# Performance work log

Hardware: AMD Instinct MI355X
Metric: run time of the kernel (lower is better)

The kernel has to match this reference:

```python
import jax, jax.numpy as jnp
import numpy as np

N_NODES = 50000
N_EDGES = 800000
IN_DIM = 128
IN_CH = 64
HIDDEN = 64
OUT_CH = 128
NUM_CLS = 16
NUM_GRAPHS = 512


def setup_inputs() -> dict:
    key = jax.random.key(0)
    ks = jax.random.split(key, 16)
    s = 0.02
    x = jax.random.normal(ks[0], (N_NODES, IN_DIM), jnp.float32)
    edge_index = jax.random.randint(ks[1], (2, N_EDGES), 0, N_NODES, jnp.int64)
    batch = jnp.sort(jax.random.randint(ks[2], (N_NODES,), 0, NUM_GRAPHS, jnp.int64))
    return {
        "x": x,
        "edge_index": edge_index,
        "batch": batch,
        "num_graphs": NUM_GRAPHS,
        "w_stage1": jax.random.normal(ks[3], (IN_DIM, IN_CH), jnp.float32) * s,
        "b_stage1": jnp.zeros((IN_CH,), jnp.float32),
        "rel1_w": jax.random.normal(ks[4], (IN_CH, HIDDEN), jnp.float32) * s,
        "rel1_b": jnp.zeros((HIDDEN,), jnp.float32),
        "root1_w": jax.random.normal(ks[5], (IN_CH, HIDDEN), jnp.float32) * s,
        "rel2_w": jax.random.normal(ks[6], (HIDDEN, 2 * HIDDEN), jnp.float32) * s,
        "rel2_b": jnp.zeros((2 * HIDDEN,), jnp.float32),
        "root2_w": jax.random.normal(ks[7], (HIDDEN, 2 * HIDDEN), jnp.float32) * s,
        "rel3_w": jax.random.normal(ks[8], (2 * HIDDEN, OUT_CH), jnp.float32) * s,
        "rel3_b": jnp.zeros((OUT_CH,), jnp.float32),
        "root3_w": jax.random.normal(ks[9], (2 * HIDDEN, OUT_CH), jnp.float32) * s,
        "lin_w": jax.random.normal(ks[10], (OUT_CH, NUM_CLS), jnp.float32) * s,
        "lin_b": jnp.zeros((NUM_CLS,), jnp.float32),
    }


def graph_conv(x, src, dst, rel_w, rel_b, root_w, n_nodes):
    # PyG GraphConv(aggr='add'): lin_rel(sum_{j in N(i)} x_j) + lin_root(x_i)
    agg = jax.ops.segment_sum(x[src], dst, num_segments=n_nodes)  # [N, in]
    return agg @ rel_w + rel_b + x @ root_w


def reference(x, edge_index, batch, num_graphs,
              w_stage1, b_stage1,
              rel1_w, rel1_b, root1_w,
              rel2_w, rel2_b, root2_w,
              rel3_w, rel3_b, root3_w,
              lin_w, lin_b):
    src, dst = edge_index[0], edge_index[1]
    n = x.shape[0]
    h = x @ w_stage1 + b_stage1                                   # [N, IN_CH]
    h = jax.nn.relu(graph_conv(h, src, dst, rel1_w, rel1_b, root1_w, n))
    h = jax.nn.relu(graph_conv(h, src, dst, rel2_w, rel2_b, root2_w, n))
    h = jax.nn.relu(graph_conv(h, src, dst, rel3_w, rel3_b, root3_w, n))
    # global mean pool over graphs
    sums = jax.ops.segment_sum(h, batch, num_segments=num_graphs)  # [G, OUT_CH]
    cnt = jax.ops.segment_sum(jnp.ones((n,), h.dtype), batch, num_segments=num_graphs)
    pooled = sums / jnp.maximum(cnt, 1.0)[:, None]
    # dropout treated as identity (deterministic eval reference)
    return pooled @ lin_w + lin_b                                  # [G, NUM_CLS]
```

## Files before the change

### kernel.cpp

```cpp
#include <hip/hip_runtime.h>
#include <hip/hip_bf16.h>

#define N_NODES 50000
#define N_EDGES 800000
#define IN_DIM  128
#define IN_CH   64
#define HIDDEN  64
#define OUT_CH  128
#define NUM_CLS 16
#define NUM_G   512
#define NBUK    ((N_NODES + 255) >> 8)
#define BCAP    6144
#define EPB_A   4096

typedef __attribute__((ext_vector_type(8))) short short8;
typedef __attribute__((ext_vector_type(4))) float f32x4;

__device__ inline float bits2f(unsigned short u) {
  unsigned x = (unsigned)u << 16;
  float f;
  __builtin_memcpy(&f, &x, 4);
  return f;
}
__device__ inline unsigned short f2bits(float v) {
  __hip_bfloat16 b = __float2bfloat16(v);
  unsigned short s;
  __builtin_memcpy(&s, &b, 2);
  return s;
}
__device__ inline short8 zero8() {
  short8 z;
#pragma unroll
  for (int i = 0; i < 8; ++i) z[i] = 0;
  return z;
}
__device__ inline void acc2(float& a0, float& a1, unsigned v) {
  a0 += bits2f((unsigned short)v);
  a1 += bits2f((unsigned short)(v >> 16));
}
__device__ inline void accu4(float* a, uint4 v) {
  acc2(a[0], a[1], v.x); acc2(a[2], a[3], v.y);
  acc2(a[4], a[5], v.z); acc2(a[6], a[7], v.w);
}

__global__ __launch_bounds__(64) void k_stage1(
    const float* __restrict__ Ap, const short* __restrict__ Wa,
    const float* __restrict__ bias, unsigned short* __restrict__ outp) {
  constexpr int DIN = 128, DOUT = 64, KT = DIN / 32, CT = DOUT / 16;
  const int lane = threadIdx.x;
  const int m = lane & 15;
  const int q = lane >> 4;
  const int row = blockIdx.x * 16 + m;
  const bool ok = row < N_NODES;

  short8 afr[KT];
#pragma unroll
  for (int kt = 0; kt < KT; ++kt) {
    short8 f = zero8();
    if (ok) {
      const float* ap = Ap + (size_t)row * DIN + kt * 32 + q * 8;
      float4 x0 = *(const float4*)ap;
      float4 x1 = *(const float4*)(ap + 4);
      f[0] = (short)f2bits(x0.x); f[1] = (short)f2bits(x0.y);
      f[2] = (short)f2bits(x0.z); f[3] = (short)f2bits(x0.w);
      f[4] = (short)f2bits(x1.x); f[5] = (short)f2bits(x1.y);
      f[6] = (short)f2bits(x1.z); f[7] = (short)f2bits(x1.w);
    }
    afr[kt] = f;
  }
  const int rbase = blockIdx.x * 16;
#pragma unroll
  for (int ct = 0; ct < CT; ++ct) {
    f32x4 c = {0.f, 0.f, 0.f, 0.f};
#pragma unroll
    for (int kt = 0; kt < KT; ++kt) {
      short8 b = *(const short8*)(Wa + ((size_t)(kt * CT + ct) * 64 + lane) * 8);
      c = __builtin_amdgcn_mfma_f32_16x16x32_bf16(afr[kt], b, c, 0, 0, 0);
    }
    float bv = bias[ct * 16 + m];
#pragma unroll
    for (int r = 0; r < 4; ++r) {
      int ro = rbase + q * 4 + r;
      if (ro < N_NODES) outp[(size_t)ro * DOUT + ct * 16 + m] = f2bits(c[r] + bv);
    }
  }
}

template <int DIN, int DOUT>
__global__ __launch_bounds__(64) void k_fused(
    const unsigned short* __restrict__ h, const int* __restrict__ esrc,
    const int* __restrict__ off, const short* __restrict__ Wa,
    const short* __restrict__ Wh, const float* __restrict__ bias,
    unsigned short* __restrict__ outp) {
  constexpr int KT = DIN / 32;
  constexpr int CT = DOUT / 16;
  const int lane = threadIdx.x;
  const int m = lane & 15;
  const int q = lane >> 4;
  const int node = blockIdx.x * 16 + m;
  const bool ok = node < N_NODES;

  float acc[KT][8];
#pragma unroll
  for (int kt = 0; kt < KT; ++kt)
#pragma unroll
    for (int j = 0; j < 8; ++j) acc[kt][j] = 0.f;

  if (ok) {
    int e = off[node], end = off[node + 1];
    const unsigned short* hq = h + q * 8;
    for (; e + 2 <= end; e += 2) {
      int s0 = esrc[e], s1 = esrc[e + 1];
      const unsigned short* r0 = hq + (size_t)s0 * DIN;
      const unsigned short* r1 = hq + (size_t)s1 * DIN;
#pragma unroll
      for (int kt = 0; kt < KT; ++kt) {
        uint4 va = *(const uint4*)(r0 + kt * 32);
        uint4 vb = *(const uint4*)(r1 + kt * 32);
        accu4(acc[kt], va);
        accu4(acc[kt], vb);
      }
    }
    if (e < end) {
      const unsigned short* r0 = hq + (size_t)esrc[e] * DIN;
#pragma unroll
      for (int kt = 0; kt < KT; ++kt)
        accu4(acc[kt], *(const uint4*)(r0 + kt * 32));
    }
  }

  short8 afr[KT], hfr[KT];
#pragma unroll
  for (int kt = 0; kt < KT; ++kt) {
    short8 f;
#pragma unroll
    for (int j = 0; j < 8; ++j) f[j] = (short)f2bits(acc[kt][j]);
    afr[kt] = f;
    hfr[kt] = ok ? *(const short8*)(h + (size_t)node * DIN + kt * 32 + q * 8)
                 : zero8();
  }

  const int rbase = blockIdx.x * 16;
#pragma unroll
  for (int ct = 0; ct < CT; ++ct) {
    f32x4 c = {0.f, 0.f, 0.f, 0.f};
#pragma unroll
    for (int kt = 0; kt < KT; ++kt) {
      short8 b = *(const short8*)(Wa + ((size_t)(kt * CT + ct) * 64 + lane) * 8);
      c = __builtin_amdgcn_mfma_f32_16x16x32_bf16(afr[kt], b, c, 0, 0, 0);
      short8 bh = *(const short8*)(Wh + ((size_t)(kt * CT + ct) * 64 + lane) * 8);
      c = __builtin_amdgcn_mfma_f32_16x16x32_bf16(hfr[kt], bh, c, 0, 0, 0);
    }
    float bv = bias[ct * 16 + m];
#pragma unroll
    for (int r = 0; r < 4; ++r) {
      int row = rbase + q * 4 + r;
      if (row < N_NODES)
        outp[(size_t)row * DOUT + ct * 16 + m] = f2bits(fmaxf(c[r] + bv, 0.f));
    }
  }
}

template <int DIN, int DOUT>
__device__ inline void pack1(const float* __restrict__ W, short* __restrict__ o,
                             int t) {
  constexpr int CT = DOUT / 16;
  int j = t & 7;
  int lane = (t >> 3) & 63;
  int kc = t >> 9;
  int ct = kc % CT;
  int kt = kc / CT;
  int k = kt * 32 + (lane >> 4) * 8 + j;
  int n = ct * 16 + (lane & 15);
  o[t] = (short)f2bits(W[k * DOUT + n]);
}

__global__ __launch_bounds__(256) void k_packall(
    const float* w1, const float* r1, const float* o1, const float* r2,
    const float* o2, const float* r3, const float* o3,
    short* w1p, short* r1p, short* o1p, short* r2p, short* o2p,
    short* r3p, short* o3p) {
  int b = blockIdx.x, t = threadIdx.x;
  if      (b < 32)  pack1<128, 64>(w1, w1p, (b - 0) * 256 + t);
  else if (b < 48)  pack1<64, 64>(r1, r1p, (b - 32) * 256 + t);
  else if (b < 64)  pack1<64, 64>(o1, o1p, (b - 48) * 256 + t);
  else if (b < 96)  pack1<64, 128>(r2, r2p, (b - 64) * 256 + t);
  else if (b < 128) pack1<64, 128>(o2, o2p, (b - 96) * 256 + t);
  else if (b < 192) pack1<128, 128>(r3, r3p, (b - 128) * 256 + t);
  else              pack1<128, 128>(o3, o3p, (b - 192) * 256 + t);
}

__global__ __launch_bounds__(256) void k_bucketA(const int* __restrict__ src,
    const int* __restrict__ dst, int* __restrict__ bcnt, uint2* __restrict__ bbuf) {
  __shared__ int hist[NBUK], sbase[NBUK], lcur[NBUK];
  const int t = threadIdx.x;
  for (int i = t; i < NBUK; i += 256) { hist[i] = 0; lcur[i] = 0; }
  __syncthreads();
  const int e0 = blockIdx.x * EPB_A;
  int s_[16], d_[16];
  int cnt = 0;
#pragma unroll
  for (int k = 0; k < 16; ++k) {
    int e = e0 + k * 256 + t;
    if (e < N_EDGES) {
      s_[cnt] = src[e]; d_[cnt] = dst[e];
      atomicAdd(&hist[d_[cnt] >> 8], 1);
      cnt++;
    }
  }
  __syncthreads();
  for (int i = t; i < NBUK; i += 256) sbase[i] = atomicAdd(&bcnt[i], hist[i]);
  __syncthreads();
  for (int k = 0; k < cnt; ++k) {
    int b = d_[k] >> 8;
    int pos = sbase[b] + atomicAdd(&lcur[b], 1);
    if (pos < BCAP) bbuf[(size_t)b * BCAP + pos] = make_uint2((unsigned)s_[k], (unsigned)d_[k]);
  }
}

__global__ __launch_bounds__(256) void k_scanb(const int* __restrict__ bcnt,
    int* __restrict__ bbase, int* __restrict__ off) {
  __shared__ int s[256];
  int t = threadIdx.x;
  int v0 = (t < NBUK) ? min(bcnt[t], BCAP) : 0;
  s[t] = v0;
  __syncthreads();
  for (int st = 1; st < 256; st <<= 1) {
    int v = (t >= st) ? s[t - st] : 0;
    __syncthreads();
    s[t] += v;
    __syncthreads();
  }
  if (t < NBUK) bbase[t] = s[t] - v0;
  if (t == NBUK - 1) off[N_NODES] = s[t];
}

__global__ __launch_bounds__(256) void k_bfin(const int* __restrict__ bcnt,
    const uint2* __restrict__ bbuf, const int* __restrict__ bbase,
    int* __restrict__ off, int* __restrict__ esrc) {
  __shared__ int cnt[256], s[256], soff[256];
  const int b = blockIdx.x;
  const int t = threadIdx.x;
  cnt[t] = 0;
  __syncthreads();
  int n = min(bcnt[b], BCAP);
  for (int i = t; i < n; i += 256)
    atomicAdd(&cnt[bbuf[(size_t)b * BCAP + i].y & 255], 1);
  __syncthreads();
  int v0 = cnt[t];
  s[t] = v0;
  __syncthreads();
  for (int st = 1; st < 256; st <<= 1) {
    int v = (t >= st) ? s[t - st] : 0;
    __syncthreads();
    s[t] += v;
    __syncthreads();
  }
  int myoff = bbase[b] + s[t] - v0;
  int node = b * 256 + t;
  if (node < N_NODES) off[node] = myoff;
  soff[t] = myoff;
  cnt[t] = 0;
  __syncthreads();
  for (int i = t; i < n; i += 256) {
    uint2 p = bbuf[(size_t)b * BCAP + i];
    int l = p.y & 255;
    int r = atomicAdd(&cnt[l], 1);
    esrc[soff[l] + r] = (int)p.x;
  }
}

__device__ inline int lbound(const int* __restrict__ a, int n, int v) {
  int lo = 0, hi = n;
  while (lo < hi) {
    int m = (lo + hi) >> 1;
    if (a[m] < v) lo = m + 1; else hi = m;
  }
  return lo;
}

__global__ __launch_bounds__(128) void k_poolhead(const unsigned short* __restrict__ h3,
    const int* __restrict__ batch, const float* __restrict__ lw,
    const float* __restrict__ lb, float* __restrict__ out) {
  __shared__ float sp[128];
  int g = blockIdx.x;
  int t = threadIdx.x;
  int lo = lbound(batch, N_NODES, g);
  int hi = lbound(batch, N_NODES, g + 1);
  float a0 = 0.f, a1 = 0.f, a2 = 0.f, a3 = 0.f;
  int r = lo;
  for (; r + 4 <= hi; r += 4) {
    a0 += bits2f(h3[(size_t)(r + 0) * OUT_CH + t]);
    a1 += bits2f(h3[(size_t)(r + 1) * OUT_CH + t]);
    a2 += bits2f(h3[(size_t)(r + 2) * OUT_CH + t]);
    a3 += bits2f(h3[(size_t)(r + 3) * OUT_CH + t]);
  }
  for (; r < hi; ++r) a0 += bits2f(h3[(size_t)r * OUT_CH + t]);
  float inv = (hi > lo) ? 1.f / (float)(hi - lo) : 0.f;
  sp[t] = ((a0 + a1) + (a2 + a3)) * inv;
  __syncthreads();
  if (t < NUM_CLS) {
    float s = lb[t];
#pragma unroll
    for (int k = 0; k < OUT_CH; ++k) s = fmaf(sp[k], lw[k * NUM_CLS + t], s);
    out[g * NUM_CLS + t] = s;
  }
}

extern "C" void kernel_launch(void* const* d_in, const int* in_sizes, int n_in,
                              void* d_out, int out_size, void* d_ws, size_t ws_size,
                              hipStream_t stream) {
  const float* x      = (const float*)d_in[0];
  const int*   ei     = (const int*)d_in[1];
  const int*   batch  = (const int*)d_in[2];
  const float* w1     = (const float*)d_in[4];
  const float* b1     = (const float*)d_in[5];
  const float* rel1w  = (const float*)d_in[6];
  const float* rel1b  = (const float*)d_in[7];
  const float* root1w = (const float*)d_in[8];
  const float* rel2w  = (const float*)d_in[9];
  const float* rel2b  = (const float*)d_in[10];
  const float* root2w = (const float*)d_in[11];
  const float* rel3w  = (const float*)d_in[12];
  const float* rel3b  = (const float*)d_in[13];
  const float* root3w = (const float*)d_in[14];
  const float* linw   = (const float*)d_in[15];
  const float* linb   = (const float*)d_in[16];
  const int* src = ei;
  const int* dst = ei + N_EDGES;
  float* out = (float*)d_out;

  unsigned short* P = (unsigned short*)d_ws;
  unsigned short* Q = P + (size_t)N_NODES * 128;
  unsigned short* R = Q + (size_t)N_NODES * 128;
  short* WP = (short*)(R + (size_t)N_NODES * 128);
  short* w1p  = WP;
  short* r1p  = w1p + 8192;
  short* o1p  = r1p + 4096;
  short* r2p  = o1p + 4096;
  short* o2p  = r2p + 8192;
  short* r3p  = o2p + 8192;
  short* o3p  = r3p + 16384;
  int* off     = (int*)(o3p + 16384);
  int* bcnt    = off + (N_NODES + 1);
  int* bbase   = bcnt + NBUK;
  int* esrc    = bbase + NBUK + 2;
  uint2* bbuf  = (uint2*)((char*)(esrc + N_EDGES) +
                          ((16 - (((size_t)(esrc + N_EDGES)) & 15)) & 15));

  hipMemsetAsync(bcnt, 0, NBUK * sizeof(int), stream);
  k_bucketA<<<(N_EDGES + EPB_A - 1) / EPB_A, 256, 0, stream>>>(src, dst, bcnt, bbuf);
  k_scanb<<<1, 256, 0, stream>>>(bcnt, bbase, off);
  k_bfin<<<NBUK, 256, 0, stream>>>(bcnt, bbuf, bbase, off, esrc);

  k_packall<<<256, 256, 0, stream>>>(w1, rel1w, root1w, rel2w, root2w, rel3w,
                                     root3w, w1p, r1p, o1p, r2p, o2p, r3p, o3p);

  const int GF = (N_NODES + 15) / 16;

  k_stage1<<<GF, 64, 0, stream>>>(x, w1p, b1, P);
  k_fused<64, 64><<<GF, 64, 0, stream>>>(P, esrc, off, r1p, o1p, rel1b, R);
  k_fused<64, 128><<<GF, 64, 0, stream>>>(R, esrc, off, r2p, o2p, rel2b, Q);
  k_fused<128, 128><<<GF, 64, 0, stream>>>(Q, esrc, off, r3p, o3p, rel3b, P);
  k_poolhead<<<NUM_G, 128, 0, stream>>>(P, batch, linw, linb, out);
}
```

Baseline: 254.8 us.

## Fold weight packing into bucketing and bucket scan into finalize kernel

Weight packing work is spread across the edge-bucketing kernel's threads, and the separate single-block bucket-prefix-scan kernel is removed. Each finalize block now recomputes the bucket scan redundantly. Together this drops two kernel launches and their serialization gaps, at the cost of redundant scan work per block and extra per-thread work in the bucketing kernel.

```diff
diff --git a/kernel.cpp b/kernel.cpp
--- a/kernel.cpp
+++ b/kernel.cpp
@@ -175,25 +175,33 @@
   o[t] = (short)f2bits(W[k * DOUT + n]);
 }
 
-__global__ __launch_bounds__(256) void k_packall(
-    const float* w1, const float* r1, const float* o1, const float* r2,
-    const float* o2, const float* r3, const float* o3,
-    short* w1p, short* r1p, short* o1p, short* r2p, short* o2p,
-    short* r3p, short* o3p) {
-  int b = blockIdx.x, t = threadIdx.x;
-  if      (b < 32)  pack1<128, 64>(w1, w1p, (b - 0) * 256 + t);
-  else if (b < 48)  pack1<64, 64>(r1, r1p, (b - 32) * 256 + t);
-  else if (b < 64)  pack1<64, 64>(o1, o1p, (b - 48) * 256 + t);
-  else if (b < 96)  pack1<64, 128>(r2, r2p, (b - 64) * 256 + t);
-  else if (b < 128) pack1<64, 128>(o2, o2p, (b - 96) * 256 + t);
-  else if (b < 192) pack1<128, 128>(r3, r3p, (b - 128) * 256 + t);
-  else              pack1<128, 128>(o3, o3p, (b - 192) * 256 + t);
+struct PackArgs {
+  const float *w1, *r1, *o1, *r2, *o2, *r3, *o3;
+  short *w1p, *r1p, *o1p, *r2p, *o2p, *r3p, *o3p;
+};
+
+__device__ inline void packflat(const PackArgs& a, int t) {
+  if      (t < 8192)  pack1<128, 64>(a.w1, a.w1p, t);
+  else if (t < 12288) pack1<64, 64>(a.r1, a.r1p, t - 8192);
+  else if (t < 16384) pack1<64, 64>(a.o1, a.o1p, t - 12288);
+  else if (t < 24576) pack1<64, 128>(a.r2, a.r2p, t - 16384);
+  else if (t < 32768) pack1<64, 128>(a.o2, a.o2p, t - 24576);
+  else if (t < 49152) pack1<128, 128>(a.r3, a.r3p, t - 32768);
+  else if (t < 65536) pack1<128, 128>(a.o3, a.o3p, t - 49152);
 }
 
 __global__ __launch_bounds__(256) void k_bucketA(const int* __restrict__ src,
-    const int* __restrict__ dst, int* __restrict__ bcnt, uint2* __restrict__ bbuf) {
+    const int* __restrict__ dst, int* __restrict__ bcnt, uint2* __restrict__ bbuf,
+    PackArgs pk) {
   __shared__ int hist[NBUK], sbase[NBUK], lcur[NBUK];
   const int t = threadIdx.x;
+
+  {
+    int g0 = blockIdx.x * 256 + t;
+    packflat(pk, g0);
+    packflat(pk, g0 + 50176);
+  }
+
   for (int i = t; i < NBUK; i += 256) { hist[i] = 0; lcur[i] = 0; }
   __syncthreads();
   const int e0 = blockIdx.x * EPB_A;
@@ -218,12 +226,15 @@
   }
 }
 
-__global__ __launch_bounds__(256) void k_scanb(const int* __restrict__ bcnt,
-    int* __restrict__ bbase, int* __restrict__ off) {
-  __shared__ int s[256];
-  int t = threadIdx.x;
-  int v0 = (t < NBUK) ? min(bcnt[t], BCAP) : 0;
-  s[t] = v0;
+__global__ __launch_bounds__(256) void k_bfin(const int* __restrict__ bcnt,
+    const uint2* __restrict__ bbuf, int* __restrict__ off,
+    int* __restrict__ esrc) {
+  __shared__ int cnt[256], s[256], soff[256];
+  const int b = blockIdx.x;
+  const int t = threadIdx.x;
+
+  int bv0 = (t < NBUK) ? min(bcnt[t], BCAP) : 0;
+  s[t] = bv0;
   __syncthreads();
   for (int st = 1; st < 256; st <<= 1) {
     int v = (t >= st) ? s[t - st] : 0;
@@ -231,16 +242,12 @@
     s[t] += v;
     __syncthreads();
   }
-  if (t < NBUK) bbase[t] = s[t] - v0;
-  if (t == NBUK - 1) off[N_NODES] = s[t];
-}
-
-__global__ __launch_bounds__(256) void k_bfin(const int* __restrict__ bcnt,
-    const uint2* __restrict__ bbuf, const int* __restrict__ bbase,
-    int* __restrict__ off, int* __restrict__ esrc) {
-  __shared__ int cnt[256], s[256], soff[256];
-  const int b = blockIdx.x;
-  const int t = threadIdx.x;
+  __shared__ int bbase_s;
+  if (t == b) bbase_s = s[t] - bv0;
+  if (b == 0 && t == NBUK - 1) off[N_NODES] = s[t];
+  __syncthreads();
+  const int bb = bbase_s;
+
   cnt[t] = 0;
   __syncthreads();
   int n = min(bcnt[b], BCAP);
@@ -256,7 +263,7 @@
     s[t] += v;
     __syncthreads();
   }
-  int myoff = bbase[b] + s[t] - v0;
+  int myoff = bb + s[t] - v0;
   int node = b * 256 + t;
   if (node < N_NODES) off[node] = myoff;
   soff[t] = myoff;
@@ -343,18 +350,17 @@
   short* o3p  = r3p + 16384;
   int* off     = (int*)(o3p + 16384);
   int* bcnt    = off + (N_NODES + 1);
-  int* bbase   = bcnt + NBUK;
-  int* esrc    = bbase + NBUK + 2;
+  int* esrc    = bcnt + NBUK + 3;
   uint2* bbuf  = (uint2*)((char*)(esrc + N_EDGES) +
                           ((16 - (((size_t)(esrc + N_EDGES)) & 15)) & 15));
 
+  PackArgs pk = {w1, rel1w, root1w, rel2w, root2w, rel3w, root3w,
+                 w1p, r1p, o1p, r2p, o2p, r3p, o3p};
+
   hipMemsetAsync(bcnt, 0, NBUK * sizeof(int), stream);
-  k_bucketA<<<(N_EDGES + EPB_A - 1) / EPB_A, 256, 0, stream>>>(src, dst, bcnt, bbuf);
-  k_scanb<<<1, 256, 0, stream>>>(bcnt, bbase, off);
-  k_bfin<<<NBUK, 256, 0, stream>>>(bcnt, bbuf, bbase, off, esrc);
-
-  k_packall<<<256, 256, 0, stream>>>(w1, rel1w, root1w, rel2w, root2w, rel3w,
-                                     root3w, w1p, r1p, o1p, r2p, o2p, r3p, o3p);
+  k_bucketA<<<(N_EDGES + EPB_A - 1) / EPB_A, 256, 0, stream>>>(src, dst, bcnt,
+                                                               bbuf, pk);
+  k_bfin<<<NBUK, 256, 0, stream>>>(bcnt, bbuf, off, esrc);
 
   const int GF = (N_NODES + 15) / 16;
 
```

Result: faster. 249.7 us (-2.0%).
